# Kernel optimization log

Measured on AMD Instinct MI355X. Metric: run time of the kernel, lower is better.

The kernel has to match this reference:

```python
import jax, jax.numpy as jnp
import numpy as np

L, H, NH, NKV, HD, S, P, FF = 2, 2048, 16, 2, 128, 1024, 1024, 5632
G = NH // NKV
THETA = 1000000.0
EPS = 1e-6
SCALE = 1.0 / np.sqrt(HD).astype(np.float32)


def rms_norm(x, w):
    return x * jax.lax.rsqrt(jnp.mean(x * x, axis=-1, keepdims=True) + EPS) * w


def rotate_half(x):
    x1, x2 = jnp.split(x, 2, axis=-1)
    return jnp.concatenate([-x2, x1], axis=-1)


def setup_inputs() -> dict:
    key = jax.random.key(0)
    ks = iter(jax.random.split(key, 16))
    w = lambda shape: jax.random.normal(next(ks), shape, jnp.float32) * 0.02
    return {
        'inputs_embeds': jax.random.normal(next(ks), (1, S, H), jnp.float32),
        'position_ids': (jnp.arange(S, dtype=jnp.int32) + P)[None, :],
        'past_k': jax.random.normal(next(ks), (L, 1, NKV, P, HD), jnp.float32),
        'past_v': jax.random.normal(next(ks), (L, 1, NKV, P, HD), jnp.float32),
        'ln1_w': jnp.ones((L, H), jnp.float32),
        'wq': w((L, H, NH * HD)), 'bq': jnp.zeros((L, NH * HD), jnp.float32),
        'wk': w((L, H, NKV * HD)), 'bk': jnp.zeros((L, NKV * HD), jnp.float32),
        'wv': w((L, H, NKV * HD)), 'bv': jnp.zeros((L, NKV * HD), jnp.float32),
        'wo': w((L, NH * HD, H)),
        'ln2_w': jnp.ones((L, H), jnp.float32),
        'w_gate': w((L, H, FF)), 'w_up': w((L, H, FF)), 'w_down': w((L, FF, H)),
        'norm_w': jnp.ones((H,), jnp.float32),
    }


def reference(inputs_embeds, position_ids, past_k, past_v, ln1_w, wq, bq, wk, bk,
              wv, bv, wo, ln2_w, w_gate, w_up, w_down, norm_w):
    pos = position_ids.astype(jnp.float32)                      # [1,S]
    inv_freq = 1.0 / (THETA ** (jnp.arange(0, HD, 2, dtype=jnp.float32) / HD))
    freqs = pos[:, :, None] * inv_freq                          # [1,S,HD/2]
    emb = jnp.concatenate([freqs, freqs], axis=-1)              # [1,S,HD]
    cos = jnp.cos(emb)[:, None]                                 # [1,1,S,HD]
    sin = jnp.sin(emb)[:, None]
    T = P + S
    k_pos = jnp.arange(T, dtype=jnp.float32)
    # causal mask over absolute positions: future keys masked with -65504
    mask = jnp.where(k_pos[None, None, None, :] > pos[:, None, :, None],
                     jnp.float32(-65504.0), jnp.float32(0.0))   # [1,1,S,T]

    hidden = inputs_embeds
    present = []
    for i in range(L):
        residual = hidden
        h = rms_norm(hidden, ln1_w[i])
        q = (h @ wq[i] + bq[i]).reshape(1, S, NH, HD).transpose(0, 2, 1, 3)
        k = (h @ wk[i] + bk[i]).reshape(1, S, NKV, HD).transpose(0, 2, 1, 3)
        v = (h @ wv[i] + bv[i]).reshape(1, S, NKV, HD).transpose(0, 2, 1, 3)
        q = q * cos + rotate_half(q) * sin
        k = k * cos + rotate_half(k) * sin
        k = jnp.concatenate([past_k[i], k], axis=2)             # [1,NKV,T,HD]
        v = jnp.concatenate([past_v[i], v], axis=2)
        present.append(k)
        present.append(v)
        # GQA: group query heads per kv head instead of expanding k/v
        qg = q.reshape(1, NKV, G, S, HD)
        attn = jnp.einsum('bkgsd,bktd->bkgst', qg, k) * SCALE   # [1,NKV,G,S,T]
        attn = jax.nn.softmax(attn + mask[:, :, None], axis=-1)
        out = jnp.einsum('bkgst,bktd->bkgsd', attn, v)
        out = out.reshape(1, NH, S, HD).transpose(0, 2, 1, 3).reshape(1, S, H)
        hidden = residual + out @ wo[i]
        residual = hidden
        h = rms_norm(hidden, ln2_w[i])
        h = (jax.nn.silu(h @ w_gate[i]) * (h @ w_up[i])) @ w_down[i]
        hidden = residual + h
    hidden = rms_norm(hidden, norm_w)
    return (hidden, *present)
```

## Files before the change

### kernel.cpp

```cpp
#include <hip/hip_runtime.h>

#define L_ 2
#define H_ 2048
#define NH_ 16
#define NKV_ 2
#define HD_ 128
#define S_ 1024
#define P_ 1024
#define T_ 2048
#define FF_ 5632
#define QKVN_ 2560
#define KOFF_ 2048
#define VOFF_ 2304

#define EPS_ 1e-6f
#define SCALE_ 0.08838834764831845f
#define DEFER_THR_ 8.0f

typedef __bf16 bf16_t;
typedef unsigned int u32;
typedef __bf16 bx8 __attribute__((ext_vector_type(8)));
typedef __bf16 bx4 __attribute__((ext_vector_type(4)));
typedef float  fx4 __attribute__((ext_vector_type(4)));

__device__ __forceinline__ fx4 mfma16(bx8 a, bx8 b, fx4 c) {
  return __builtin_amdgcn_mfma_f32_16x16x32_bf16(a, b, c, 0, 0, 0);
}

#define GLL16(gsrc, ldst) __builtin_amdgcn_global_load_lds( \
    (__attribute__((address_space(1))) void*)(gsrc),        \
    (__attribute__((address_space(3))) void*)(ldst), 16, 0, 0)

__device__ __forceinline__ bx8 lds_read_b128(char* p) {
  u32 a = (u32)(uintptr_t)(__attribute__((address_space(3))) void*)p;
  bx8 d;
  asm volatile("ds_read_b128 %0, %1" : "=v"(d) : "v"(a));
  return d;
}
__device__ __forceinline__ void lds_write_b16(char* p, float v) {
  u32 a = (u32)(uintptr_t)(__attribute__((address_space(3))) void*)p;
  bf16_t b = (bf16_t)v;
  u32 d = (u32)__builtin_bit_cast(unsigned short, b);
  asm volatile("ds_write_b16 %0, %1" :: "v"(a), "v"(d));
}

#define LGKM(n) asm volatile("s_waitcnt lgkmcnt(" #n ")" ::: "memory"); __builtin_amdgcn_sched_barrier(0)

__device__ __forceinline__ int xcd_swizzle(int orig, int nwg) {
  int q = nwg >> 3, r = nwg & 7;
  int xcd = orig & 7, lid = orig >> 3;
  return (xcd < r ? xcd * (q + 1) : r * (q + 1) + (xcd - r) * q) + lid;
}

__global__ void k_rope_tables(const int* __restrict__ pos, float* __restrict__ ct, float* __restrict__ st) {
  int i = blockIdx.x * 256 + threadIdx.x;
  if (i >= S_ * 64) return;
  int s = i >> 6, d = i & 63;
  float p = (float)pos[s];
  float inv = expf(-(float)(2 * d) * (13.815510557964274f / 128.0f));
  float f = p * inv;
  ct[i] = cosf(f);
  st[i] = sinf(f);
}

__global__ void k_copy4(const float* __restrict__ in, float* __restrict__ out, int n4) {
  int i = blockIdx.x * 256 + threadIdx.x;
  if (i < n4) ((fx4*)out)[i] = ((const fx4*)in)[i];
}

__global__ void k_cbias(const float* __restrict__ bq, const float* __restrict__ bk,
                        const float* __restrict__ bv, float* __restrict__ cb) {
  int i = blockIdx.x * 256 + threadIdx.x;
  if (i >= L_ * QKVN_) return;
  int l = i / QKVN_, j = i % QKVN_;
  float v;
  if (j < KOFF_)      v = bq[l * KOFF_ + j];
  else if (j < VOFF_) v = bk[l * (NKV_ * HD_) + j - KOFF_];
  else                v = bv[l * (NKV_ * HD_) + j - VOFF_];
  cb[i] = v;
}

template<int OUTBF>
__global__ __launch_bounds__(256) void k_rmsnorm(const float* __restrict__ x, const float* __restrict__ w,
                                                 void* __restrict__ y) {
  int row = blockIdx.x, tid = threadIdx.x;
  const fx4* xr = (const fx4*)(x + (size_t)row * H_);
  fx4 v0 = xr[tid], v1 = xr[tid + 256];
  float ss = v0[0]*v0[0] + v0[1]*v0[1] + v0[2]*v0[2] + v0[3]*v0[3]
           + v1[0]*v1[0] + v1[1]*v1[1] + v1[2]*v1[2] + v1[3]*v1[3];
  #pragma unroll
  for (int off = 32; off > 0; off >>= 1) ss += __shfl_xor(ss, off);
  __shared__ float red[4];
  if ((tid & 63) == 0) red[tid >> 6] = ss;
  __syncthreads();
  float tot = red[0] + red[1] + red[2] + red[3];
  float rs = rsqrtf(tot * (1.0f / H_) + EPS_);
  const fx4* wr_ = (const fx4*)w;
  fx4 w0 = wr_[tid], w1 = wr_[tid + 256];
  if (OUTBF) {
    bf16_t* yb = (bf16_t*)y + (size_t)row * H_;
    bx4 o0, o1;
    #pragma unroll
    for (int i = 0; i < 4; i++) { o0[i] = (bf16_t)(v0[i] * rs * w0[i]); o1[i] = (bf16_t)(v1[i] * rs * w1[i]); }
    *(bx4*)&yb[tid * 4] = o0;
    *(bx4*)&yb[(tid + 256) * 4] = o1;
  } else {
    float* yf = (float*)y + (size_t)row * H_;
    fx4 o0, o1;
    #pragma unroll
    for (int i = 0; i < 4; i++) { o0[i] = v0[i] * rs * w0[i]; o1[i] = v1[i] * rs * w1[i]; }
    *(fx4*)&yf[tid * 4] = o0;
    *(fx4*)&yf[(tid + 256) * 4] = o1;
  }
}

__global__ __launch_bounds__(256) void k_transpose_w(const float* __restrict__ in, bf16_t* __restrict__ out,
                                                     int R, int C) {
  __shared__ __attribute__((aligned(16))) float Tt[64 * 68];
  int tid = threadIdx.x;
  int c0 = blockIdx.x * 64, r0 = blockIdx.y * 64;
  #pragma unroll
  for (int j = 0; j < 4; j++) {
    int c = j * 256 + tid;
    int row = c >> 4, col = (c & 15) * 4;
    *(fx4*)&Tt[row * 68 + col] = *(const fx4*)&in[(size_t)(r0 + row) * C + c0 + col];
  }
  __syncthreads();
  #pragma unroll
  for (int j = 0; j < 2; j++) {
    int c = j * 256 + tid;
    int n = c >> 3, ko = (c & 7) * 8;
    bx8 o;
    #pragma unroll
    for (int i = 0; i < 8; i++) o[i] = (bf16_t)Tt[(ko + i) * 68 + n];
    *(bx8*)&out[(size_t)(c0 + n) * R + r0 + ko] = o;
  }
}

template<int OUTBF, int HASB, int HASR, int HASG, int SPLIT>
__global__ __launch_bounds__(256) void k_gemm(const bf16_t* __restrict__ A, const bf16_t* __restrict__ Bt,
                                              const float* __restrict__ bias, const float* __restrict__ res,
                                              const bf16_t* __restrict__ gmul,
                                              void* __restrict__ out, int M, int N, int lda, int kLen, int gy) {
  __shared__ __attribute__((aligned(16))) bf16_t sA[2][64 * 64];
  __shared__ __attribute__((aligned(16))) bf16_t sB[2][128 * 64];
  int tid = threadIdx.x;
  int w = tid >> 6, lane = tid & 63, g = lane >> 4, r = lane & 15;
  int wr = w >> 1, wc = w & 1;
  int swzid = xcd_swizzle((int)blockIdx.x, (int)gridDim.x);
  int per = (int)gridDim.x / SPLIT;
  int sp = swzid / per;
  int rem = swzid - sp * per;
  int m0 = (rem % gy) * 64;
  int n0 = (rem / gy) * 128;
  A  += (size_t)sp * kLen;
  Bt += (size_t)sp * kLen;
  fx4 acc[2][4] = {};
  int swz = (r & 7) << 4;
  int col0 = (g * 16) ^ swz;
  int col1 = (64 + g * 16) ^ swz;
  int wbase = (tid & ~63) * 16;
  int nk = kLen >> 6;

  auto STAGE = [&](int buf, int k0) {
    #pragma unroll
    for (int j = 0; j < 2; j++) {
      int d = (j * 256 + tid) * 16;
      int row = d >> 7;
      int inrow = (d & 127) ^ ((row & 7) << 4);
      GLL16((const char*)(A + (size_t)(m0 + row) * lda + k0) + inrow,
            (char*)&sA[buf][0] + j * 4096 + wbase);
    }
    #pragma unroll
    for (int j = 0; j < 4; j++) {
      int d = (j * 256 + tid) * 16;
      int row = d >> 7;
      int inrow = (d & 127) ^ ((row & 7) << 4);
      GLL16((const char*)(Bt + (size_t)(n0 + row) * lda + k0) + inrow,
            (char*)&sB[buf][0] + j * 4096 + wbase);
    }
  };

  STAGE(0, 0);
  int cur = 0;
  for (int t = 0; t < nk; t++) {
    if (t + 1 < nk) {
      STAGE(cur ^ 1, (t + 1) << 6);
      asm volatile("s_waitcnt vmcnt(6)" ::: "memory");
    } else {
      asm volatile("s_waitcnt vmcnt(0)" ::: "memory");
    }
    __builtin_amdgcn_s_barrier();
    __builtin_amdgcn_sched_barrier(0);
    char* pa = (char*)&sA[cur][0] + (wr * 32 + r) * 128;
    char* pb = (char*)&sB[cur][0] + (wc * 64 + r) * 128;
    bx8 fa[2][2], fb[4][2];
    fa[0][0] = lds_read_b128(pa + col0);
    fa[1][0] = lds_read_b128(pa + 2048 + col0);
    #pragma unroll
    for (int n = 0; n < 4; n++) fb[n][0] = lds_read_b128(pb + n * 2048 + col0);
    fa[0][1] = lds_read_b128(pa + col1);
    fa[1][1] = lds_read_b128(pa + 2048 + col1);
    #pragma unroll
    for (int n = 0; n < 4; n++) fb[n][1] = lds_read_b128(pb + n * 2048 + col1);
    LGKM(6);
    __builtin_amdgcn_s_setprio(1);
    #pragma unroll
    for (int n = 0; n < 4; n++) {
      acc[0][n] = mfma16(fa[0][0], fb[n][0], acc[0][n]);
      acc[1][n] = mfma16(fa[1][0], fb[n][0], acc[1][n]);
    }
    __builtin_amdgcn_s_setprio(0);
    LGKM(0);
    __builtin_amdgcn_s_setprio(1);
    #pragma unroll
    for (int n = 0; n < 4; n++) {
      acc[0][n] = mfma16(fa[0][1], fb[n][1], acc[0][n]);
      acc[1][n] = mfma16(fa[1][1], fb[n][1], acc[1][n]);
    }
    __builtin_amdgcn_s_setprio(0);
    if (t + 1 < nk) {
      __builtin_amdgcn_s_barrier();
      __builtin_amdgcn_sched_barrier(0);
    }
    cur ^= 1;
  }
  #pragma unroll
  for (int m = 0; m < 2; m++)
    #pragma unroll
    for (int n = 0; n < 4; n++) {
      int col = n0 + wc * 64 + n * 16 + r;
      #pragma unroll
      for (int rr = 0; rr < 4; rr++) {
        int row = m0 + wr * 32 + m * 16 + 4 * g + rr;
        float v = acc[m][n][rr];
        if (SPLIT > 1) {
          atomicAdd(&((float*)out)[(size_t)row * N + col], v);
        } else {
          if (HASB) v += bias[col];
          if (HASR) v += res[(size_t)row * N + col];
          if (HASG) {
            float x = (float)gmul[(size_t)row * N + col];
            v = (x / (1.0f + __expf(-x))) * v;
          }
          if (OUTBF) ((bf16_t*)out)[(size_t)row * N + col] = (bf16_t)v;
          else       ((float*)out)[(size_t)row * N + col] = v;
        }
      }
    }
}

template<int OUTBF, int HASG, int SPLIT>
__global__ __launch_bounds__(256) void k_gemm_big(const bf16_t* __restrict__ A, const bf16_t* __restrict__ Bt,
                                                  const bf16_t* __restrict__ gmul,
                                                  void* __restrict__ out, int M, int N, int lda, int kLen, int gy) {
  __shared__ __attribute__((aligned(16))) bf16_t sA[2][128 * 64];
  __shared__ __attribute__((aligned(16))) bf16_t sB[2][128 * 64];
  int tid = threadIdx.x;
  int w = tid >> 6, lane = tid & 63, g = lane >> 4, r = lane & 15;
  int wr = w >> 1, wc = w & 1;
  int swzid = xcd_swizzle((int)blockIdx.x, (int)gridDim.x);
  int per = (int)gridDim.x / SPLIT;
  int sp = swzid / per;
  int rem = swzid - sp * per;
  int m0 = (rem % gy) * 128;
  int n0 = (rem / gy) * 128;
  A  += (size_t)sp * kLen;
  Bt += (size_t)sp * kLen;
  fx4 acc[4][4] = {};
  int swz = (r & 7) << 4;
  int col0 = (g * 16) ^ swz;
  int col1 = (64 + g * 16) ^ swz;
  int wbase = (tid & ~63) * 16;
  int nk = kLen >> 6;

  auto STAGE = [&](int buf, int k0) {
    #pragma unroll
    for (int j = 0; j < 4; j++) {
      int d = (j * 256 + tid) * 16;
      int row = d >> 7;
      int inrow = (d & 127) ^ ((row & 7) << 4);
      GLL16((const char*)(A + (size_t)(m0 + row) * lda + k0) + inrow,
            (char*)&sA[buf][0] + j * 4096 + wbase);
    }
    #pragma unroll
    for (int j = 0; j < 4; j++) {
      int d = (j * 256 + tid) * 16;
      int row = d >> 7;
      int inrow = (d & 127) ^ ((row & 7) << 4);
      GLL16((const char*)(Bt + (size_t)(n0 + row) * lda + k0) + inrow,
            (char*)&sB[buf][0] + j * 4096 + wbase);
    }
  };

  STAGE(0, 0);
  int cur = 0;
  for (int t = 0; t < nk; t++) {
    if (t + 1 < nk) {
      STAGE(cur ^ 1, (t + 1) << 6);
      asm volatile("s_waitcnt vmcnt(8)" ::: "memory");
    } else {
      asm volatile("s_waitcnt vmcnt(0)" ::: "memory");
    }
    __builtin_amdgcn_s_barrier();
    __builtin_amdgcn_sched_barrier(0);
    char* pa = (char*)&sA[cur][0] + (wr * 64 + r) * 128;
    char* pb = (char*)&sB[cur][0] + (wc * 64 + r) * 128;
    bx8 fa[4][2], fb[4][2];
    #pragma unroll
    for (int m = 0; m < 4; m++) fa[m][0] = lds_read_b128(pa + m * 2048 + col0);
    #pragma unroll
    for (int n = 0; n < 4; n++) fb[n][0] = lds_read_b128(pb + n * 2048 + col0);
    #pragma unroll
    for (int m = 0; m < 4; m++) fa[m][1] = lds_read_b128(pa + m * 2048 + col1);
    #pragma unroll
    for (int n = 0; n < 4; n++) fb[n][1] = lds_read_b128(pb + n * 2048 + col1);
    LGKM(8);
    __builtin_amdgcn_s_setprio(1);
    #pragma unroll
    for (int m = 0; m < 4; m++)
      #pragma unroll
      for (int n = 0; n < 4; n++)
        acc[m][n] = mfma16(fa[m][0], fb[n][0], acc[m][n]);
    __builtin_amdgcn_s_setprio(0);
    LGKM(0);
    __builtin_amdgcn_s_setprio(1);
    #pragma unroll
    for (int m = 0; m < 4; m++)
      #pragma unroll
      for (int n = 0; n < 4; n++)
        acc[m][n] = mfma16(fa[m][1], fb[n][1], acc[m][n]);
    __builtin_amdgcn_s_setprio(0);
    if (t + 1 < nk) {
      __builtin_amdgcn_s_barrier();
      __builtin_amdgcn_sched_barrier(0);
    }
    cur ^= 1;
  }
  #pragma unroll
  for (int m = 0; m < 4; m++)
    #pragma unroll
    for (int n = 0; n < 4; n++) {
      int col = n0 + wc * 64 + n * 16 + r;
      #pragma unroll
      for (int rr = 0; rr < 4; rr++) {
        int row = m0 + wr * 64 + m * 16 + 4 * g + rr;
        float v = acc[m][n][rr];
        if (SPLIT > 1) {
          atomicAdd(&((float*)out)[(size_t)row * N + col], v);
        } else {
          if (HASG) {
            float x = (float)gmul[(size_t)row * N + col];
            v = (x / (1.0f + __expf(-x))) * v;
          }
          if (OUTBF) ((bf16_t*)out)[(size_t)row * N + col] = (bf16_t)v;
          else       ((float*)out)[(size_t)row * N + col] = v;
        }
      }
    }
}

__global__ void k_rope_q(const bf16_t* __restrict__ qkv, const float* __restrict__ ct,
                         const float* __restrict__ st, bf16_t* __restrict__ qout) {
  int i = blockIdx.x * 256 + threadIdx.x;
  if (i >= S_ * NH_ * 64) return;
  int d = i & 63, h = (i >> 6) & 15, s = i >> 10;
  size_t ib = (size_t)s * QKVN_ + h * HD_;
  float x1 = (float)qkv[ib + d];
  float x2 = (float)qkv[ib + d + 64];
  float c = ct[s * 64 + d], sn = st[s * 64 + d];
  size_t ob = ((size_t)h * S_ + s) * HD_;
  qout[ob + d]      = (bf16_t)(x1 * c - x2 * sn);
  qout[ob + d + 64] = (bf16_t)(x2 * c + x1 * sn);
}

__global__ void k_build_k(const bf16_t* __restrict__ qkv, const float* __restrict__ pastk,
                          const float* __restrict__ ct, const float* __restrict__ st,
                          bf16_t* __restrict__ kc, float* __restrict__ pk_out) {
  int i = blockIdx.x * 256 + threadIdx.x;
  if (i >= NKV_ * T_ * 64) return;
  int d = i & 63, t = (i >> 6) & (T_ - 1), kv = i >> 17;
  size_t cb = ((size_t)kv * T_ + t) * HD_;
  if (t < P_) {
    size_t pb = ((size_t)kv * P_ + t) * HD_;
    float a = pastk[pb + d], b = pastk[pb + d + 64];
    kc[cb + d] = (bf16_t)a; kc[cb + d + 64] = (bf16_t)b;
    pk_out[cb + d] = a;     pk_out[cb + d + 64] = b;
  } else {
    int s = t - P_;
    size_t ib = (size_t)s * QKVN_ + KOFF_ + kv * HD_;
    float x1 = (float)qkv[ib + d];
    float x2 = (float)qkv[ib + d + 64];
    float c = ct[s * 64 + d], sn = st[s * 64 + d];
    float k1 = x1 * c - x2 * sn, k2 = x2 * c + x1 * sn;
    kc[cb + d] = (bf16_t)k1; kc[cb + d + 64] = (bf16_t)k2;
    pk_out[cb + d] = k1;     pk_out[cb + d + 64] = k2;
  }
}

__global__ __launch_bounds__(256) void k_build_vt(const bf16_t* __restrict__ qkv, const float* __restrict__ pastv,
                                                  bf16_t* __restrict__ vt, float* __restrict__ pv_out) {
  int t0 = blockIdx.x * 64, d0 = blockIdx.y * 64, kv = blockIdx.z;
  __shared__ __attribute__((aligned(16))) float Tt[64 * 68];
  int tid = threadIdx.x;
  if (t0 < P_) {
    #pragma unroll
    for (int j = 0; j < 4; j++) {
      int c = j * 256 + tid;
      int row = c >> 4, col = (c & 15) * 4;
      int t = t0 + row;
      fx4 v = *(const fx4*)&pastv[((size_t)kv * P_ + t) * HD_ + d0 + col];
      *(fx4*)&Tt[row * 68 + col] = v;
      *(fx4*)&pv_out[((size_t)kv * T_ + t) * HD_ + d0 + col] = v;
    }
  } else {
    #pragma unroll
    for (int j = 0; j < 4; j++) {
      int c = j * 256 + tid;
      int row = c >> 4, col = (c & 15) * 4;
      int t = t0 + row;
      bx4 b = *(const bx4*)&qkv[(size_t)(t - P_) * QKVN_ + VOFF_ + kv * HD_ + d0 + col];
      fx4 v;
      #pragma unroll
      for (int q = 0; q < 4; q++) v[q] = (float)b[q];
      *(fx4*)&Tt[row * 68 + col] = v;
      *(fx4*)&pv_out[((size_t)kv * T_ + t) * HD_ + d0 + col] = v;
    }
  }
  __syncthreads();
  #pragma unroll
  for (int j = 0; j < 2; j++) {
    int c = j * 256 + tid;
    int n = c >> 3, ko = (c & 7) * 8;
    bx8 o;
    #pragma unroll
    for (int i = 0; i < 8; i++) o[i] = (bf16_t)Tt[(ko + i) * 68 + n];
    *(bx8*)&vt[((size_t)kv * HD_ + d0 + n) * T_ + t0 + ko] = o;
  }
}

__global__ __launch_bounds__(128) void k_attn(const bf16_t* __restrict__ Q, const bf16_t* __restrict__ Kc,
                                              const bf16_t* __restrict__ VT, bf16_t* __restrict__ O) {
  __shared__ __attribute__((aligned(16))) bf16_t Klds[2][64 * 128];
  __shared__ __attribute__((aligned(16))) bf16_t Vlds[2][128 * 64];
  __shared__ __attribute__((aligned(16))) bf16_t Plds[2][16][72];
  int tid = threadIdx.x;
  int w = tid >> 6, lane = tid & 63, g = lane >> 4, r = lane & 15;
  int b = blockIdx.x;
  int half = b >> 8;
  int idx = b & 255;
  int cx = idx & 31;
  int chunk = half ? (31 - cx) : cx;
  int h = (half << 3) | (idx >> 5);
  int kv = half;
  int m0 = chunk * 32;
  int qr0 = m0 + w * 16;
  const bf16_t* qb = Q + ((size_t)h * S_ + qr0 + r) * HD_ + g * 8;
  bx8 qf[4];
  #pragma unroll
  for (int kc = 0; kc < 4; kc++) qf[kc] = *(const bx8*)(qb + kc * 32);
  fx4 of[8] = {};
  float mrun[4], lrun[4];
  #pragma unroll
  for (int i = 0; i < 4; i++) { mrun[i] = -1e30f; lrun[i] = 0.0f; }
  int lim = P_ + qr0 + 4 * g;
  int ntile = (P_ + m0 + 32 + 63) >> 6;
  const char* kg = (const char*)(Kc + (size_t)kv * T_ * HD_);
  const char* vg = (const char*)(VT + (size_t)kv * HD_ * T_);
  int wbase = (tid & ~63) * 16;

  auto STAGE = [&](int buf, int t0) {
    #pragma unroll
    for (int j = 0; j < 8; j++) {
      int D = j * 2048 + tid * 16;
      int row = D >> 8, inrow = D & 255;
      const char* src = kg + (size_t)(t0 + row) * 256 + (inrow ^ ((row & 7) << 4));
      GLL16(src, (char*)&Klds[buf][0] + j * 2048 + wbase);
    }
    #pragma unroll
    for (int j = 0; j < 8; j++) {
      int D = j * 2048 + tid * 16;
      int row = D >> 7, inrow = D & 127;
      const char* src = vg + (size_t)row * 4096 + (size_t)t0 * 2 + (inrow ^ ((row & 7) << 4));
      GLL16(src, (char*)&Vlds[buf][0] + j * 2048 + wbase);
    }
  };

  STAGE(0, 0);
  asm volatile("s_waitcnt vmcnt(0)" ::: "memory");
  __builtin_amdgcn_s_barrier();
  __builtin_amdgcn_sched_barrier(0);
  int cur = 0;
  for (int t = 0; t < ntile; t++) {
    int t0 = t * 64;
    if (t + 1 < ntile) {
      STAGE(cur ^ 1, t0 + 64);
      asm volatile("s_waitcnt vmcnt(16)" ::: "memory");
    } else {
      asm volatile("s_waitcnt vmcnt(0)" ::: "memory");
    }
    __builtin_amdgcn_s_barrier();
    __builtin_amdgcn_sched_barrier(0);
    char* kb = (char*)&Klds[cur][0];
    char* vb = (char*)&Vlds[cur][0];
    bx8 kf[4][4];
    #pragma unroll
    for (int nt = 0; nt < 4; nt++) {
      int row = nt * 16 + r;
      char* kr = kb + row * 256;
      int sz = (row & 7) << 4;
      #pragma unroll
      for (int kc = 0; kc < 4; kc++)
        kf[nt][kc] = lds_read_b128(kr + (((kc * 32 + g * 8) * 2) ^ sz));
    }
    fx4 sc[4] = {};
    LGKM(12);
    #pragma unroll
    for (int kc = 0; kc < 4; kc++) sc[0] = mfma16(qf[kc], kf[0][kc], sc[0]);
    LGKM(8);
    #pragma unroll
    for (int kc = 0; kc < 4; kc++) sc[1] = mfma16(qf[kc], kf[1][kc], sc[1]);
    LGKM(4);
    #pragma unroll
    for (int kc = 0; kc < 4; kc++) sc[2] = mfma16(qf[kc], kf[2][kc], sc[2]);
    LGKM(0);
    #pragma unroll
    for (int kc = 0; kc < 4; kc++) sc[3] = mfma16(qf[kc], kf[3][kc], sc[3]);
    bx8 vf0[8], vf1[8];
    #pragma unroll
    for (int dt = 0; dt < 8; dt++) {
      int row = dt * 16 + r;
      vf0[dt] = lds_read_b128(vb + row * 128 + (((g * 8) * 2) ^ ((row & 7) << 4)));
    }
    #pragma unroll
    for (int dt = 0; dt < 8; dt++) {
      int row = dt * 16 + r;
      vf1[dt] = lds_read_b128(vb + row * 128 + (((32 + g * 8) * 2) ^ ((row & 7) << 4)));
    }
    float lm[4] = {-1e30f, -1e30f, -1e30f, -1e30f};
    #pragma unroll
    for (int nt = 0; nt < 4; nt++)
      #pragma unroll
      for (int rr = 0; rr < 4; rr++) {
        int key = t0 + nt * 16 + r;
        float sv = sc[nt][rr] * SCALE_;
        sv = (key > lim + rr) ? -1e30f : sv;
        sc[nt][rr] = sv;
        lm[rr] = fmaxf(lm[rr], sv);
      }
    int ok = (lm[0] <= mrun[0] + DEFER_THR_) & (lm[1] <= mrun[1] + DEFER_THR_) &
             (lm[2] <= mrun[2] + DEFER_THR_) & (lm[3] <= mrun[3] + DEFER_THR_);
    if (!__all(ok)) {
      float av[4];
      #pragma unroll
      for (int off = 1; off < 16; off <<= 1)
        #pragma unroll
        for (int rr = 0; rr < 4; rr++) lm[rr] = fmaxf(lm[rr], __shfl_xor(lm[rr], off));
      #pragma unroll
      for (int rr = 0; rr < 4; rr++) {
        float mn = fmaxf(mrun[rr], lm[rr]);
        av[rr] = __expf(mrun[rr] - mn);
        mrun[rr] = mn;
        lrun[rr] *= av[rr];
      }
      #pragma unroll
      for (int f = 0; f < 8; f++)
        #pragma unroll
        for (int rr = 0; rr < 4; rr++) of[f][rr] *= av[rr];
    }
    #pragma unroll
    for (int nt = 0; nt < 2; nt++)
      #pragma unroll
      for (int rr = 0; rr < 4; rr++) {
        float pr = __expf(sc[nt][rr] - mrun[rr]);
        lrun[rr] += pr;
        lds_write_b16((char*)&Plds[w][4 * g + rr][nt * 16 + r], pr);
      }
    bx8 pa0 = lds_read_b128((char*)&Plds[w][r][g * 8]);
    #pragma unroll
    for (int nt = 2; nt < 4; nt++)
      #pragma unroll
      for (int rr = 0; rr < 4; rr++) {
        float pr = __expf(sc[nt][rr] - mrun[rr]);
        lrun[rr] += pr;
        lds_write_b16((char*)&Plds[w][4 * g + rr][nt * 16 + r], pr);
      }
    bx8 pa1 = lds_read_b128((char*)&Plds[w][r][32 + g * 8]);
    LGKM(9);
    #pragma unroll
    for (int dt = 0; dt < 8; dt++) of[dt] = mfma16(pa0, vf0[dt], of[dt]);
    LGKM(0);
    #pragma unroll
    for (int dt = 0; dt < 8; dt++) of[dt] = mfma16(pa1, vf1[dt], of[dt]);
    __builtin_amdgcn_s_barrier();
    cur ^= 1;
  }
  #pragma unroll
  for (int off = 1; off < 16; off <<= 1)
    #pragma unroll
    for (int rr = 0; rr < 4; rr++) lrun[rr] += __shfl_xor(lrun[rr], off);
  float li[4];
  #pragma unroll
  for (int rr = 0; rr < 4; rr++) li[rr] = 1.0f / lrun[rr];
  #pragma unroll
  for (int dt = 0; dt < 8; dt++)
    #pragma unroll
    for (int rr = 0; rr < 4; rr++)
      O[(size_t)(qr0 + 4 * g + rr) * H_ + h * HD_ + dt * 16 + r] = (bf16_t)(of[dt][rr] * li[rr]);
}

extern "C" void kernel_launch(void* const* d_in, const int* in_sizes, int n_in,
                              void* d_out, int out_size, void* d_ws, size_t ws_size,
                              hipStream_t stream) {
  const float* embeds = (const float*)d_in[0];
  const int*   pos    = (const int*)d_in[1];
  const float* past_k = (const float*)d_in[2];
  const float* past_v = (const float*)d_in[3];
  const float* ln1    = (const float*)d_in[4];
  const float* wq     = (const float*)d_in[5];
  const float* bq     = (const float*)d_in[6];
  const float* wk     = (const float*)d_in[7];
  const float* bk     = (const float*)d_in[8];
  const float* wv     = (const float*)d_in[9];
  const float* bv     = (const float*)d_in[10];
  const float* wo     = (const float*)d_in[11];
  const float* ln2    = (const float*)d_in[12];
  const float* wg     = (const float*)d_in[13];
  const float* wu     = (const float*)d_in[14];
  const float* wd     = (const float*)d_in[15];
  const float* normw  = (const float*)d_in[16];

  char* wsp = (char*)d_ws;
  auto take = [&](size_t n) { char* p = wsp; wsp += (n + 255) & ~(size_t)255; return (void*)p; };
  float*  cos_t  = (float*)take((size_t)S_ * 64 * 4);
  float*  sin_t  = (float*)take((size_t)S_ * 64 * 4);
  float*  cbias  = (float*)take((size_t)L_ * QKVN_ * 4);
  float*  hidden = (float*)take((size_t)S_ * H_ * 4);
  bf16_t* hnorm  = (bf16_t*)take((size_t)S_ * H_ * 2);
  bf16_t* qkv    = (bf16_t*)take((size_t)S_ * QKVN_ * 2);
  bf16_t* qrope  = (bf16_t*)take((size_t)NH_ * S_ * HD_ * 2);
  bf16_t* kcache = (bf16_t*)take((size_t)NKV_ * T_ * HD_ * 2);
  bf16_t* vtr    = (bf16_t*)take((size_t)NKV_ * HD_ * T_ * 2);
  bf16_t* attno  = (bf16_t*)take((size_t)S_ * H_ * 2);
  bf16_t* gateb  = (bf16_t*)take((size_t)S_ * FF_ * 2);
  bf16_t* hgb    = (bf16_t*)take((size_t)S_ * FF_ * 2);
  bf16_t* wT     = (bf16_t*)take((size_t)FF_ * H_ * 2);

  float* out_h = (float*)d_out;

  k_rope_tables<<<256, 256, 0, stream>>>(pos, cos_t, sin_t);
  k_cbias<<<(L_ * QKVN_ + 255) / 256, 256, 0, stream>>>(bq, bk, bv, cbias);
  k_copy4<<<(S_ * H_ / 4 + 255) / 256, 256, 0, stream>>>(embeds, hidden, S_ * H_ / 4);

  for (int l = 0; l < L_; l++) {
    const float* wq_l = wq + (size_t)l * H_ * (NH_ * HD_);
    const float* wk_l = wk + (size_t)l * H_ * (NKV_ * HD_);
    const float* wv_l = wv + (size_t)l * H_ * (NKV_ * HD_);
    const float* wo_l = wo + (size_t)l * (NH_ * HD_) * H_;
    const float* wg_l = wg + (size_t)l * H_ * FF_;
    const float* wu_l = wu + (size_t)l * H_ * FF_;
    const float* wd_l = wd + (size_t)l * FF_ * H_;
    const float* pk_in = past_k + (size_t)l * NKV_ * P_ * HD_;
    const float* pv_in = past_v + (size_t)l * NKV_ * P_ * HD_;
    float* pk_out = out_h + (size_t)S_ * H_ + (size_t)l * 2 * NKV_ * T_ * HD_;
    float* pv_out = pk_out + (size_t)NKV_ * T_ * HD_;

    k_rmsnorm<1><<<S_, 256, 0, stream>>>(hidden, ln1 + (size_t)l * H_, hnorm);
    k_transpose_w<<<dim3(32, 32), 256, 0, stream>>>(wq_l, wT, H_, NH_ * HD_);
    k_transpose_w<<<dim3(4, 32), 256, 0, stream>>>(wk_l, wT + (size_t)KOFF_ * H_, H_, NKV_ * HD_);
    k_transpose_w<<<dim3(4, 32), 256, 0, stream>>>(wv_l, wT + (size_t)VOFF_ * H_, H_, NKV_ * HD_);
    k_gemm<1, 1, 0, 0, 1><<<(QKVN_ / 128) * (S_ / 64), 256, 0, stream>>>(
        hnorm, wT, cbias + (size_t)l * QKVN_, nullptr, nullptr, qkv, S_, QKVN_, H_, H_, S_ / 64);
    k_rope_q<<<(S_ * NH_ * 64) / 256, 256, 0, stream>>>(qkv, cos_t, sin_t, qrope);
    k_build_k<<<(NKV_ * T_ * 64) / 256, 256, 0, stream>>>(qkv, pk_in, cos_t, sin_t, kcache, pk_out);
    k_build_vt<<<dim3(T_ / 64, HD_ / 64, NKV_), 256, 0, stream>>>(qkv, pv_in, vtr, pv_out);
    k_attn<<<512, 128, 0, stream>>>(qrope, kcache, vtr, attno);
    k_transpose_w<<<dim3(32, 32), 256, 0, stream>>>(wo_l, wT, NH_ * HD_, H_);
    k_gemm<0, 0, 0, 0, 2><<<2 * (H_ / 128) * (S_ / 64), 256, 0, stream>>>(
        attno, wT, nullptr, nullptr, nullptr, hidden, S_, H_, NH_ * HD_, (NH_ * HD_) / 2, S_ / 64);
    k_rmsnorm<1><<<S_, 256, 0, stream>>>(hidden, ln2 + (size_t)l * H_, hnorm);
    k_transpose_w<<<dim3(88, 32), 256, 0, stream>>>(wg_l, wT, H_, FF_);
    k_gemm_big<1, 0, 1><<<(FF_ / 128) * (S_ / 128), 256, 0, stream>>>(
        hnorm, wT, nullptr, gateb, S_, FF_, H_, H_, S_ / 128);
    k_transpose_w<<<dim3(88, 32), 256, 0, stream>>>(wu_l, wT, H_, FF_);
    k_gemm_big<1, 1, 1><<<(FF_ / 128) * (S_ / 128), 256, 0, stream>>>(
        hnorm, wT, gateb, hgb, S_, FF_, H_, H_, S_ / 128);
    k_transpose_w<<<dim3(32, 88), 256, 0, stream>>>(wd_l, wT, FF_, H_);
    k_gemm_big<0, 0, 2><<<2 * (H_ / 128) * (S_ / 128), 256, 0, stream>>>(
        hgb, wT, nullptr, hidden, S_, H_, FF_, FF_ / 2, S_ / 128);
  }
  k_rmsnorm<0><<<S_, 256, 0, stream>>>(hidden, normw, out_h);
}
```

Baseline: 558.8 us.

## Fuse gate and up projections into one GEMM with SwiGLU epilogue

Replaces the separate gate GEMM (which wrote a bf16 gate buffer) and the up GEMM (which reread it) with one kernel. The new kernel stages A once and both transposed weight tiles, keeps two accumulator sets, and applies SiLU(gate)*up in the epilogue. This removes the intermediate gate buffer round trip and one pass over A. The wo projection switches from split-K atomics to a single pass with a fused residual add. The down projection moves from the 128x128 big-tile kernel to the 64-row k_gemm with split-K of 2. The fused kernel uses a smaller M tile (64 rows) and more LDS, and needs a second transposed-weight buffer.

```diff
diff --git a/kernel.cpp b/kernel.cpp
--- a/kernel.cpp
+++ b/kernel.cpp
@@ -250,33 +250,28 @@
     }
 }
 
-template<int OUTBF, int HASG, int SPLIT>
-__global__ __launch_bounds__(256) void k_gemm_big(const bf16_t* __restrict__ A, const bf16_t* __restrict__ Bt,
-                                                  const bf16_t* __restrict__ gmul,
-                                                  void* __restrict__ out, int M, int N, int lda, int kLen, int gy) {
-  __shared__ __attribute__((aligned(16))) bf16_t sA[2][128 * 64];
-  __shared__ __attribute__((aligned(16))) bf16_t sB[2][128 * 64];
+__global__ __launch_bounds__(256) void k_gemm_gu(const bf16_t* __restrict__ A, const bf16_t* __restrict__ Bg,
+                                                 const bf16_t* __restrict__ Bu, bf16_t* __restrict__ out,
+                                                 int M, int N, int lda, int gy) {
+  __shared__ __attribute__((aligned(16))) bf16_t sA[2][64 * 64];
+  __shared__ __attribute__((aligned(16))) bf16_t sBg[2][128 * 64];
+  __shared__ __attribute__((aligned(16))) bf16_t sBu[2][128 * 64];
   int tid = threadIdx.x;
   int w = tid >> 6, lane = tid & 63, g = lane >> 4, r = lane & 15;
   int wr = w >> 1, wc = w & 1;
   int swzid = xcd_swizzle((int)blockIdx.x, (int)gridDim.x);
-  int per = (int)gridDim.x / SPLIT;
-  int sp = swzid / per;
-  int rem = swzid - sp * per;
-  int m0 = (rem % gy) * 128;
-  int n0 = (rem / gy) * 128;
-  A  += (size_t)sp * kLen;
-  Bt += (size_t)sp * kLen;
-  fx4 acc[4][4] = {};
+  int m0 = (swzid % gy) * 64;
+  int n0 = (swzid / gy) * 128;
+  fx4 accg[2][4] = {}, accu[2][4] = {};
   int swz = (r & 7) << 4;
   int col0 = (g * 16) ^ swz;
   int col1 = (64 + g * 16) ^ swz;
   int wbase = (tid & ~63) * 16;
-  int nk = kLen >> 6;
+  int nk = lda >> 6;
 
   auto STAGE = [&](int buf, int k0) {
     #pragma unroll
-    for (int j = 0; j < 4; j++) {
+    for (int j = 0; j < 2; j++) {
       int d = (j * 256 + tid) * 16;
       int row = d >> 7;
       int inrow = (d & 127) ^ ((row & 7) << 4);
@@ -288,8 +283,16 @@
       int d = (j * 256 + tid) * 16;
       int row = d >> 7;
       int inrow = (d & 127) ^ ((row & 7) << 4);
-      GLL16((const char*)(Bt + (size_t)(n0 + row) * lda + k0) + inrow,
-            (char*)&sB[buf][0] + j * 4096 + wbase);
+      GLL16((const char*)(Bg + (size_t)(n0 + row) * lda + k0) + inrow,
+            (char*)&sBg[buf][0] + j * 4096 + wbase);
+    }
+    #pragma unroll
+    for (int j = 0; j < 4; j++) {
+      int d = (j * 256 + tid) * 16;
+      int row = d >> 7;
+      int inrow = (d & 127) ^ ((row & 7) << 4);
+      GLL16((const char*)(Bu + (size_t)(n0 + row) * lda + k0) + inrow,
+            (char*)&sBu[buf][0] + j * 4096 + wbase);
     }
   };
 
@@ -298,38 +301,47 @@
   for (int t = 0; t < nk; t++) {
     if (t + 1 < nk) {
       STAGE(cur ^ 1, (t + 1) << 6);
-      asm volatile("s_waitcnt vmcnt(8)" ::: "memory");
+      asm volatile("s_waitcnt vmcnt(10)" ::: "memory");
     } else {
       asm volatile("s_waitcnt vmcnt(0)" ::: "memory");
     }
     __builtin_amdgcn_s_barrier();
     __builtin_amdgcn_sched_barrier(0);
-    char* pa = (char*)&sA[cur][0] + (wr * 64 + r) * 128;
-    char* pb = (char*)&sB[cur][0] + (wc * 64 + r) * 128;
-    bx8 fa[4][2], fb[4][2];
-    #pragma unroll
-    for (int m = 0; m < 4; m++) fa[m][0] = lds_read_b128(pa + m * 2048 + col0);
-    #pragma unroll
-    for (int n = 0; n < 4; n++) fb[n][0] = lds_read_b128(pb + n * 2048 + col0);
-    #pragma unroll
-    for (int m = 0; m < 4; m++) fa[m][1] = lds_read_b128(pa + m * 2048 + col1);
-    #pragma unroll
-    for (int n = 0; n < 4; n++) fb[n][1] = lds_read_b128(pb + n * 2048 + col1);
-    LGKM(8);
+    char* pa = (char*)&sA[cur][0] + (wr * 32 + r) * 128;
+    char* pg = (char*)&sBg[cur][0] + (wc * 64 + r) * 128;
+    char* pu = (char*)&sBu[cur][0] + (wc * 64 + r) * 128;
+    bx8 fa[2][2], fg[4][2], fu[4][2];
+    fa[0][0] = lds_read_b128(pa + col0);
+    fa[1][0] = lds_read_b128(pa + 2048 + col0);
+    #pragma unroll
+    for (int n = 0; n < 4; n++) fg[n][0] = lds_read_b128(pg + n * 2048 + col0);
+    #pragma unroll
+    for (int n = 0; n < 4; n++) fu[n][0] = lds_read_b128(pu + n * 2048 + col0);
+    fa[0][1] = lds_read_b128(pa + col1);
+    fa[1][1] = lds_read_b128(pa + 2048 + col1);
+    #pragma unroll
+    for (int n = 0; n < 4; n++) fg[n][1] = lds_read_b128(pg + n * 2048 + col1);
+    #pragma unroll
+    for (int n = 0; n < 4; n++) fu[n][1] = lds_read_b128(pu + n * 2048 + col1);
+    LGKM(10);
     __builtin_amdgcn_s_setprio(1);
     #pragma unroll
-    for (int m = 0; m < 4; m++)
-      #pragma unroll
-      for (int n = 0; n < 4; n++)
-        acc[m][n] = mfma16(fa[m][0], fb[n][0], acc[m][n]);
+    for (int n = 0; n < 4; n++) {
+      accg[0][n] = mfma16(fa[0][0], fg[n][0], accg[0][n]);
+      accg[1][n] = mfma16(fa[1][0], fg[n][0], accg[1][n]);
+      accu[0][n] = mfma16(fa[0][0], fu[n][0], accu[0][n]);
+      accu[1][n] = mfma16(fa[1][0], fu[n][0], accu[1][n]);
+    }
     __builtin_amdgcn_s_setprio(0);
     LGKM(0);
     __builtin_amdgcn_s_setprio(1);
     #pragma unroll
-    for (int m = 0; m < 4; m++)
-      #pragma unroll
-      for (int n = 0; n < 4; n++)
-        acc[m][n] = mfma16(fa[m][1], fb[n][1], acc[m][n]);
+    for (int n = 0; n < 4; n++) {
+      accg[0][n] = mfma16(fa[0][1], fg[n][1], accg[0][n]);
+      accg[1][n] = mfma16(fa[1][1], fg[n][1], accg[1][n]);
+      accu[0][n] = mfma16(fa[0][1], fu[n][1], accu[0][n]);
+      accu[1][n] = mfma16(fa[1][1], fu[n][1], accu[1][n]);
+    }
     __builtin_amdgcn_s_setprio(0);
     if (t + 1 < nk) {
       __builtin_amdgcn_s_barrier();
@@ -338,24 +350,17 @@
     cur ^= 1;
   }
   #pragma unroll
-  for (int m = 0; m < 4; m++)
+  for (int m = 0; m < 2; m++)
     #pragma unroll
     for (int n = 0; n < 4; n++) {
       int col = n0 + wc * 64 + n * 16 + r;
       #pragma unroll
       for (int rr = 0; rr < 4; rr++) {
-        int row = m0 + wr * 64 + m * 16 + 4 * g + rr;
-        float v = acc[m][n][rr];
-        if (SPLIT > 1) {
-          atomicAdd(&((float*)out)[(size_t)row * N + col], v);
-        } else {
-          if (HASG) {
-            float x = (float)gmul[(size_t)row * N + col];
-            v = (x / (1.0f + __expf(-x))) * v;
-          }
-          if (OUTBF) ((bf16_t*)out)[(size_t)row * N + col] = (bf16_t)v;
-          else       ((float*)out)[(size_t)row * N + col] = v;
-        }
+        int row = m0 + wr * 32 + m * 16 + 4 * g + rr;
+        float x = accg[m][n][rr];
+        float u = accu[m][n][rr];
+        float s = x / (1.0f + __expf(-x));
+        out[(size_t)row * N + col] = (bf16_t)(s * u);
       }
     }
 }
@@ -642,9 +647,9 @@
   bf16_t* kcache = (bf16_t*)take((size_t)NKV_ * T_ * HD_ * 2);
   bf16_t* vtr    = (bf16_t*)take((size_t)NKV_ * HD_ * T_ * 2);
   bf16_t* attno  = (bf16_t*)take((size_t)S_ * H_ * 2);
-  bf16_t* gateb  = (bf16_t*)take((size_t)S_ * FF_ * 2);
   bf16_t* hgb    = (bf16_t*)take((size_t)S_ * FF_ * 2);
   bf16_t* wT     = (bf16_t*)take((size_t)FF_ * H_ * 2);
+  bf16_t* wTu    = (bf16_t*)take((size_t)FF_ * H_ * 2);
 
   float* out_h = (float*)d_out;
 
@@ -676,18 +681,16 @@
     k_build_vt<<<dim3(T_ / 64, HD_ / 64, NKV_), 256, 0, stream>>>(qkv, pv_in, vtr, pv_out);
     k_attn<<<512, 128, 0, stream>>>(qrope, kcache, vtr, attno);
     k_transpose_w<<<dim3(32, 32), 256, 0, stream>>>(wo_l, wT, NH_ * HD_, H_);
-    k_gemm<0, 0, 0, 0, 2><<<2 * (H_ / 128) * (S_ / 64), 256, 0, stream>>>(
-        attno, wT, nullptr, nullptr, nullptr, hidden, S_, H_, NH_ * HD_, (NH_ * HD_) / 2, S_ / 64);
+    k_gemm<0, 0, 1, 0, 1><<<(H_ / 128) * (S_ / 64), 256, 0, stream>>>(
+        attno, wT, nullptr, hidden, nullptr, hidden, S_, H_, NH_ * HD_, NH_ * HD_, S_ / 64);
     k_rmsnorm<1><<<S_, 256, 0, stream>>>(hidden, ln2 + (size_t)l * H_, hnorm);
     k_transpose_w<<<dim3(88, 32), 256, 0, stream>>>(wg_l, wT, H_, FF_);
-    k_gemm_big<1, 0, 1><<<(FF_ / 128) * (S_ / 128), 256, 0, stream>>>(
-        hnorm, wT, nullptr, gateb, S_, FF_, H_, H_, S_ / 128);
-    k_transpose_w<<<dim3(88, 32), 256, 0, stream>>>(wu_l, wT, H_, FF_);
-    k_gemm_big<1, 1, 1><<<(FF_ / 128) * (S_ / 128), 256, 0, stream>>>(
-        hnorm, wT, gateb, hgb, S_, FF_, H_, H_, S_ / 128);
+    k_transpose_w<<<dim3(88, 32), 256, 0, stream>>>(wu_l, wTu, H_, FF_);
+    k_gemm_gu<<<(FF_ / 128) * (S_ / 64), 256, 0, stream>>>(
+        hnorm, wT, wTu, hgb, S_, FF_, H_, S_ / 64);
     k_transpose_w<<<dim3(32, 88), 256, 0, stream>>>(wd_l, wT, FF_, H_);
-    k_gemm_big<0, 0, 2><<<2 * (H_ / 128) * (S_ / 128), 256, 0, stream>>>(
-        hgb, wT, nullptr, hidden, S_, H_, FF_, FF_ / 2, S_ / 128);
+    k_gemm<0, 0, 0, 0, 2><<<2 * (H_ / 128) * (S_ / 64), 256, 0, stream>>>(
+        hgb, wT, nullptr, nullptr, nullptr, hidden, S_, H_, FF_, FF_ / 2, S_ / 64);
   }
   k_rmsnorm<0><<<S_, 256, 0, stream>>>(hidden, normw, out_h);
 }
```

Result: faster. 544.4 us (-2.6%).
